# Optimization experiments

Hardware: AMD Instinct MI355X
Metric: run time of the kernel (lower is better)

The kernel has to match this reference:

```python
import jax, jax.numpy as jnp
import numpy as np

D_MODEL = 1024
NUM_HEADS = 16
HEAD_DIM = D_MODEL // NUM_HEADS
NUM_KERNELS = 21


def tisa_bias(amp, off, sharp, seq_len):
    # amp/off/sharp: (H, K). Returns (H, L, L) translation-invariant bias.
    # Evaluate on the 2L-1 distinct relative distances, then gather (Toeplitz).
    d = jnp.arange(-(seq_len - 1), seq_len, dtype=amp.dtype)  # (2L-1,)
    # (H, K, 2L-1) -> sum over kernels -> (H, 2L-1)
    scores = jnp.sum(
        amp[:, :, None]
        * jnp.exp(-jnp.abs(sharp)[:, :, None] * (d[None, None, :] - off[:, :, None]) ** 2),
        axis=1,
    )
    i = jnp.arange(seq_len)
    rel_idx = i[None, :] - i[:, None] + (seq_len - 1)  # (L, L) in [0, 2L-2]
    return scores[:, rel_idx]  # (H, L, L)


def setup_inputs() -> dict:
    key = jax.random.key(0)
    ks = jax.random.split(key, 9)
    B, L = 4, 1024
    s = 0.02
    return {
        "x_q": jax.random.normal(ks[0], (B, L, D_MODEL), dtype=jnp.float32),
        "x_kv": jax.random.normal(ks[1], (B, L, D_MODEL), dtype=jnp.float32),
        "Wq": jax.random.normal(ks[2], (D_MODEL, D_MODEL), dtype=jnp.float32) * s,
        "Wm": jax.random.normal(ks[3], (D_MODEL, 2 * D_MODEL), dtype=jnp.float32) * s,
        "Wg": jax.random.normal(ks[4], (D_MODEL, 2 * D_MODEL), dtype=jnp.float32) * s,
        "bg": jnp.zeros((2 * D_MODEL,), dtype=jnp.float32),
        "tisa_amp": jax.random.normal(ks[5], (NUM_HEADS, NUM_KERNELS), dtype=jnp.float32) * 0.1,
        "tisa_off": jax.random.uniform(ks[6], (NUM_HEADS, NUM_KERNELS), dtype=jnp.float32, minval=-512.0, maxval=512.0),
        "tisa_sharp": jax.random.uniform(ks[7], (NUM_HEADS, NUM_KERNELS), dtype=jnp.float32, minval=1e-4, maxval=0.05),
    }


def reference(x_q, x_kv, Wq, Wm, Wg, bg, tisa_amp, tisa_off, tisa_sharp):
    B, Lq, _ = x_q.shape
    Lkv = x_kv.shape[1]
    H, Dh = NUM_HEADS, HEAD_DIM

    q = (x_q @ Wq).reshape(B, Lq, H, Dh).transpose(0, 2, 1, 3)        # (B,H,Lq,Dh)
    mem = (x_kv @ Wm)                                                 # (B,Lkv,2D)
    k = mem[..., :D_MODEL].reshape(B, Lkv, H, Dh).transpose(0, 2, 1, 3)
    v = mem[..., D_MODEL:].reshape(B, Lkv, H, Dh).transpose(0, 2, 1, 3)

    scale = 1.0 / jnp.sqrt(jnp.asarray(Dh, dtype=q.dtype))
    scores = jnp.einsum("bhqd,bhkd->bhqk", q, k) * scale              # (B,H,Lq,Lkv)
    scores = scores + tisa_bias(tisa_amp, tisa_off, tisa_sharp, Lkv)[None]
    weights = jax.nn.softmax(scores, axis=-1)

    attn = jnp.einsum("bhqk,bhkd->bhqd", weights, v)                  # (B,H,Lq,Dh)
    attn = attn.transpose(0, 2, 1, 3).reshape(B, Lq, D_MODEL)

    g = attn @ Wg + bg                                                # (B,Lq,2D)
    a, b = g[..., :D_MODEL], g[..., D_MODEL:]
    return a * jax.nn.sigmoid(b)
```

## Files before the change

kernel.cpp:

```cpp
#include <hip/hip_runtime.h>
#include <cstdint>
#include <cstddef>

typedef __attribute__((ext_vector_type(8))) short bf16x8;
typedef __attribute__((ext_vector_type(4))) float f32x4;

#define LOG2E 1.44269504f

__device__ __forceinline__ unsigned short f2bf(float x) {
  unsigned int u = __float_as_uint(x);
  u += 0x7FFFu + ((u >> 16) & 1u);
  return (unsigned short)(u >> 16);
}
__device__ __forceinline__ unsigned short f2bf_trunc(float x) {
  return (unsigned short)(__float_as_uint(x) >> 16);
}

__device__ __forceinline__ void gload_lds16(const void* g, void* l) {
  __builtin_amdgcn_global_load_lds(
      (const __attribute__((address_space(1))) unsigned int*)g,
      (__attribute__((address_space(3))) unsigned int*)l, 16, 0, 0);
}


__global__ void preproc(const float* __restrict__ x_q, const float* __restrict__ x_kv,
                        const float* __restrict__ Wq, const float* __restrict__ Wm,
                        const float* __restrict__ Wg,
                        const float* __restrict__ amp, const float* __restrict__ off,
                        const float* __restrict__ sharp,
                        ushort4* __restrict__ bXq, ushort4* __restrict__ bXkv,
                        unsigned short* __restrict__ dWq, unsigned short* __restrict__ dWm,
                        unsigned short* __restrict__ dWg, float* __restrict__ tab) {
  __shared__ float tile[32][33];
  const int blk = blockIdx.x;
  if (blk < 8192) {
    int i = blk * 256 + threadIdx.x;
    float4 v;
    ushort4* d;
    if (i < (1 << 20)) { v = ((const float4*)x_q)[i]; d = bXq + i; }
    else { int j = i - (1 << 20); v = ((const float4*)x_kv)[j]; d = bXkv + j; }
    ushort4 o;
    o.x = f2bf(v.x); o.y = f2bf(v.y); o.z = f2bf(v.z); o.w = f2bf(v.w);
    *d = o;
  } else if (blk < 14336) {
    int idx = blk - 8192;
    int z = idx >> 11, rem = idx & 2047;
    int bx = rem & 63, by = rem >> 6;
    const float* src = z == 0 ? Wq : (z == 1 ? Wm : Wg);
    unsigned short* dst = z == 0 ? dWq : (z == 1 ? dWm : dWg);
    int N = z == 0 ? 1024 : 2048;
    int nb = bx * 32, kb = by * 32;
    if (nb >= N) return;
    int tx = threadIdx.x & 31, ty = threadIdx.x >> 5;
#pragma unroll
    for (int r = ty; r < 32; r += 8)
      tile[r][tx] = src[(size_t)(kb + r) * N + nb + tx];
    __syncthreads();
#pragma unroll
    for (int r = ty; r < 32; r += 8)
      dst[(size_t)(nb + r) * 1024 + kb + tx] = f2bf(tile[tx][r]);
  } else {
    int h = blk - 14336;
    for (int idx = threadIdx.x; idx < 2047; idx += 256) {
      float d = (float)(idx - 1023);
      float acc = 0.f;
#pragma unroll
      for (int k = 0; k < 21; ++k) {
        float dd = d - off[h * 21 + k];
        acc += amp[h * 21 + k] * __expf(-fabsf(sharp[h * 21 + k]) * dd * dd);
      }
      tab[h * 2047 + idx] = acc * LOG2E;
    }
  }
}


__global__ __launch_bounds__(256)
void qkv_gemm(const unsigned short* __restrict__ Xq,
              const unsigned short* __restrict__ Xkv,
              const unsigned short* __restrict__ WqT,
              const unsigned short* __restrict__ WmT,
              unsigned short* __restrict__ qbuf,
              unsigned short* __restrict__ kbuf,
              unsigned short* __restrict__ vtbuf) {
  __shared__ unsigned short sA[2][128 * 32];
  __shared__ unsigned short sB[2][128 * 32];
  const int bx = blockIdx.y;
  const bool isQ = bx < 8;
  const int ntile = (isQ ? bx : bx - 8) << 7;
  const unsigned short* A = isQ ? Xq : Xkv;
  const unsigned short* B = (isQ ? WqT : WmT) + (size_t)ntile * 1024;
  const int t = threadIdx.x, lane = t & 63, w = t >> 6;
  const int wm = (w >> 1) << 6, wn = (w & 1) << 6;
  const int mtile = blockIdx.x << 7;
  const int c = lane & 15, g = lane >> 4;
  const int srow = t >> 2, scol = (t & 3) << 3;
  const unsigned short* aP = A + (size_t)(mtile + srow) * 1024 + scol;
  const unsigned short* bP = B + (size_t)srow * 1024 + scol;
  const int lo = srow * 32 + scol;

  gload_lds16(aP, &sA[0][lo]);
  gload_lds16(aP + 64 * 1024, &sA[0][lo + 64 * 32]);
  gload_lds16(bP, &sB[0][lo]);
  gload_lds16(bP + 64 * 1024, &sB[0][lo + 64 * 32]);
  __syncthreads();

  f32x4 acc[4][4] = {};
  for (int kt = 0; kt < 32; ++kt) {
    const int cur = kt & 1;
    if (kt + 1 < 32) {
      const int ko = (kt + 1) * 32;
      gload_lds16(aP + ko, &sA[1 - cur][lo]);
      gload_lds16(aP + 64 * 1024 + ko, &sA[1 - cur][lo + 64 * 32]);
      gload_lds16(bP + ko, &sB[1 - cur][lo]);
      gload_lds16(bP + 64 * 1024 + ko, &sB[1 - cur][lo + 64 * 32]);
    }
    bf16x8 af[4], bfr[4];
#pragma unroll
    for (int i = 0; i < 4; ++i) {
      af[i]  = *(const bf16x8*)&sA[cur][(wm + i * 16 + c) * 32 + g * 8];
      bfr[i] = *(const bf16x8*)&sB[cur][(wn + i * 16 + c) * 32 + g * 8];
    }
#pragma unroll
    for (int i = 0; i < 4; ++i)
#pragma unroll
      for (int j = 0; j < 4; ++j)
        acc[i][j] = __builtin_amdgcn_mfma_f32_16x16x32_bf16(af[i], bfr[j], acc[i][j], 0, 0, 0);
    __syncthreads();
  }

  const int row0 = mtile + wm + (g << 2);
  const int col0 = ntile + wn + c;
  if (isQ) {
#pragma unroll
    for (int i = 0; i < 4; ++i)
#pragma unroll
      for (int j = 0; j < 4; ++j) {
        int r = row0 + i * 16, cl = col0 + j * 16;
#pragma unroll
        for (int ri = 0; ri < 4; ++ri)
          qbuf[(size_t)(r + ri) * 1024 + cl] = f2bf(acc[i][j][ri] * (0.125f * LOG2E));
      }
  } else {
#pragma unroll
    for (int i = 0; i < 4; ++i)
#pragma unroll
      for (int j = 0; j < 4; ++j) {
        int r = row0 + i * 16, cl = col0 + j * 16;
        if (cl < 1024) {
#pragma unroll
          for (int ri = 0; ri < 4; ++ri)
            kbuf[(size_t)(r + ri) * 1024 + cl] = f2bf(acc[i][j][ri]);
        } else {
          int d = cl - 1024;
          int hh = d >> 6, dh = d & 63;
          int bb = r >> 10, ll = r & 1023;
          ushort4 pk;
          pk.x = f2bf(acc[i][j][0]);
          pk.y = f2bf(acc[i][j][1]);
          pk.z = f2bf(acc[i][j][2]);
          pk.w = f2bf(acc[i][j][3]);
          *(ushort4*)&vtbuf[((size_t)((bb * 16 + hh) * 64 + dh) << 10) + ll] = pk;
        }
      }
  }
}


__global__ __launch_bounds__(512)
void attn_kernel(const unsigned short* __restrict__ qbuf,
                 const unsigned short* __restrict__ kbuf,
                 const unsigned short* __restrict__ vtbuf,
                 const float* __restrict__ biasTab,
                 unsigned short* __restrict__ attnb) {
  const int h = blockIdx.x & 15, b = blockIdx.x >> 4, qt = blockIdx.y;
  __shared__ unsigned short sK[2][64 * 64];
  __shared__ unsigned short sV[3][64 * 64];
  __shared__ unsigned short sP[2][128 * 64];
  __shared__ float sLsum[2][128];
  const int t = threadIdx.x, lane = t & 63, w = t >> 6;
  const int c = lane & 15, g = lane >> 4;
  const int rg = w >> 1, cg = w & 1;

  const int r = t >> 3, ch = (t & 7) ^ (r & 7);

  const unsigned short* qsrc = qbuf + (size_t)(b * 1024 + qt * 128) * 1024 + h * 64;
  const unsigned short* ksrc = kbuf + (size_t)(b * 1024) * 1024 + h * 64;
  const unsigned short* vsrc = vtbuf + (size_t)((b * 16 + h) * 64) * 1024;

  unsigned short* sQ = &sP[0][0];
  gload_lds16(qsrc + (size_t)r * 1024 + ch * 8, &sQ[t * 8]);
  gload_lds16(qsrc + (size_t)(r + 64) * 1024 + ch * 8, &sQ[4096 + t * 8]);
  gload_lds16(ksrc + (size_t)r * 1024 + ch * 8, &sK[0][t * 8]);
  gload_lds16(vsrc + (size_t)r * 1024 + ch * 8, &sV[0][t * 8]);

  const float* bb = biasTab + h * 2047 + 1023 + cg * 32 + c - qt * 128 - rg * 32 - g * 4;

  float bc[2][2][4];
#pragma unroll
  for (int rf = 0; rf < 2; ++rf)
#pragma unroll
    for (int nf = 0; nf < 2; ++nf)
#pragma unroll
      for (int ri = 0; ri < 4; ++ri)
        bc[rf][nf][ri] = bb[(nf - rf) * 16 - ri];

  __syncthreads();

  bf16x8 aq[2][2];
#pragma unroll
  for (int rf = 0; rf < 2; ++rf) {
    int row = rg * 32 + rf * 16 + c;
#pragma unroll
    for (int ks = 0; ks < 2; ++ks)
      aq[rf][ks] = *(const bf16x8*)&sQ[row * 64 + (((ks * 4 + g) ^ (row & 7)) * 8)];
  }
  __syncthreads();

  f32x4 o[2][2] = {};
  float lsum[2][4] = {};

  int vcur = 0, vnx = 1;
  for (int kv = 0; kv < 16; ++kv) {
    const int cur = kv & 1;

    f32x4 s[2][2];
#pragma unroll
    for (int rf = 0; rf < 2; ++rf)
#pragma unroll
      for (int nf = 0; nf < 2; ++nf)
#pragma unroll
        for (int ri = 0; ri < 4; ++ri)
          s[rf][nf][ri] = bc[rf][nf][ri];

    if (kv + 1 < 16) {
      gload_lds16(ksrc + (size_t)((kv + 1) * 64 + r) * 1024 + ch * 8, &sK[1 - cur][t * 8]);
      gload_lds16(vsrc + (size_t)r * 1024 + (kv + 1) * 64 + ch * 8, &sV[vnx][t * 8]);
      const float* bk = bb + (kv + 1) * 64;
#pragma unroll
      for (int rf = 0; rf < 2; ++rf)
#pragma unroll
        for (int nf = 0; nf < 2; ++nf)
#pragma unroll
          for (int ri = 0; ri < 4; ++ri)
            bc[rf][nf][ri] = bk[(nf - rf) * 16 - ri];
    }

#pragma unroll
    for (int nf = 0; nf < 2; ++nf) {
      int krow = cg * 32 + nf * 16 + c;
      bf16x8 k0 = *(const bf16x8*)&sK[cur][krow * 64 + (((g) ^ (krow & 7)) * 8)];
      bf16x8 k1 = *(const bf16x8*)&sK[cur][krow * 64 + (((4 + g) ^ (krow & 7)) * 8)];
#pragma unroll
      for (int rf = 0; rf < 2; ++rf) {
        s[rf][nf] = __builtin_amdgcn_mfma_f32_16x16x32_bf16(aq[rf][0], k0, s[rf][nf], 0, 0, 0);
        s[rf][nf] = __builtin_amdgcn_mfma_f32_16x16x32_bf16(aq[rf][1], k1, s[rf][nf], 0, 0, 0);
      }
    }

#pragma unroll
    for (int rf = 0; rf < 2; ++rf)
#pragma unroll
      for (int nf = 0; nf < 2; ++nf)
#pragma unroll
        for (int ri = 0; ri < 4; ++ri) {
          float e = exp2f(s[rf][nf][ri]);
          lsum[rf][ri] += e;
          int prow = rg * 32 + rf * 16 + g * 4 + ri;
          int chunk = cg * 4 + nf * 2 + (c >> 3);
          sP[cur][prow * 64 + ((chunk ^ (prow & 7)) * 8) + (c & 7)] = f2bf_trunc(e);
        }
    __syncthreads();

    bf16x8 ap[2][2];
#pragma unroll
    for (int rf = 0; rf < 2; ++rf) {
      int row = rg * 32 + rf * 16 + c;
#pragma unroll
      for (int ks = 0; ks < 2; ++ks)
        ap[rf][ks] = *(const bf16x8*)&sP[cur][row * 64 + (((ks * 4 + g) ^ (row & 7)) * 8)];
    }
#pragma unroll
    for (int df = 0; df < 2; ++df) {
      int vrow = cg * 32 + df * 16 + c;
      bf16x8 v0 = *(const bf16x8*)&sV[vcur][vrow * 64 + (((g) ^ (vrow & 7)) * 8)];
      bf16x8 v1 = *(const bf16x8*)&sV[vcur][vrow * 64 + (((4 + g) ^ (vrow & 7)) * 8)];
#pragma unroll
      for (int rf = 0; rf < 2; ++rf) {
        o[rf][df] = __builtin_amdgcn_mfma_f32_16x16x32_bf16(ap[rf][0], v0, o[rf][df], 0, 0, 0);
        o[rf][df] = __builtin_amdgcn_mfma_f32_16x16x32_bf16(ap[rf][1], v1, o[rf][df], 0, 0, 0);
      }
    }
    vcur = vnx;
    vnx = (vnx == 2) ? 0 : vnx + 1;
  }

#pragma unroll
  for (int off = 1; off < 16; off <<= 1)
#pragma unroll
    for (int rf = 0; rf < 2; ++rf)
#pragma unroll
      for (int ri = 0; ri < 4; ++ri)
        lsum[rf][ri] += __shfl_xor(lsum[rf][ri], off, 64);
  if (c == 0) {
#pragma unroll
    for (int rf = 0; rf < 2; ++rf)
#pragma unroll
      for (int ri = 0; ri < 4; ++ri)
        sLsum[cg][rg * 32 + rf * 16 + g * 4 + ri] = lsum[rf][ri];
  }
  __syncthreads();

  unsigned short* obase = attnb +
      (size_t)(b * 1024 + qt * 128 + rg * 32 + g * 4) * 1024 + h * 64 + cg * 32 + c;
#pragma unroll
  for (int rf = 0; rf < 2; ++rf)
#pragma unroll
    for (int ri = 0; ri < 4; ++ri) {
      int row = rg * 32 + rf * 16 + g * 4 + ri;
      float rinv = 1.0f / (sLsum[0][row] + sLsum[1][row]);
#pragma unroll
      for (int df = 0; df < 2; ++df)
        obase[(size_t)(rf * 16 + ri) * 1024 + df * 16] = f2bf(o[rf][df][ri] * rinv);
    }
}


__global__ __launch_bounds__(256, 4)
void out_gemm(const unsigned short* __restrict__ A,
              const unsigned short* __restrict__ WgT,
              const float* __restrict__ bg,
              float* __restrict__ out) {
  __shared__ unsigned short sA[2][64 * 32];
  __shared__ unsigned short sB[2][128 * 32];
  const int nb = blockIdx.y;
  const int mtile = blockIdx.x << 6;
  const int t = threadIdx.x, lane = t & 63, w = t >> 6;
  const int c = lane & 15, g = lane >> 4;
  const int rm = w >> 1, cn = w & 1;
  const int srow = t >> 2, scol = (t & 3) << 3;
  const unsigned short* aP = A + (size_t)(mtile + srow) * 1024 + scol;
  const unsigned short* bP0 = WgT + (size_t)(nb * 64 + srow) * 1024 + scol;
  const unsigned short* bP1 = WgT + (size_t)(1024 + nb * 64 + srow) * 1024 + scol;
  const int lo = srow * 32 + scol;

  gload_lds16(aP, &sA[0][lo]);
  gload_lds16(bP0, &sB[0][lo]);
  gload_lds16(bP1, &sB[0][lo + 64 * 32]);
  __syncthreads();

  f32x4 acc[2][4] = {};
  for (int kt = 0; kt < 32; ++kt) {
    const int cur = kt & 1;
    if (kt + 1 < 32) {
      const int ko = (kt + 1) * 32;
      gload_lds16(aP + ko, &sA[1 - cur][lo]);
      gload_lds16(bP0 + ko, &sB[1 - cur][lo]);
      gload_lds16(bP1 + ko, &sB[1 - cur][lo + 64 * 32]);
    }
    bf16x8 af[2], bfr[4];
#pragma unroll
    for (int i = 0; i < 2; ++i)
      af[i] = *(const bf16x8*)&sA[cur][(rm * 32 + i * 16 + c) * 32 + g * 8];
#pragma unroll
    for (int jj = 0; jj < 2; ++jj) {
      bfr[jj]     = *(const bf16x8*)&sB[cur][(cn * 32 + jj * 16 + c) * 32 + g * 8];
      bfr[jj + 2] = *(const bf16x8*)&sB[cur][(64 + cn * 32 + jj * 16 + c) * 32 + g * 8];
    }
#pragma unroll
    for (int i = 0; i < 2; ++i)
#pragma unroll
      for (int j = 0; j < 4; ++j)
        acc[i][j] = __builtin_amdgcn_mfma_f32_16x16x32_bf16(af[i], bfr[j], acc[i][j], 0, 0, 0);
    __syncthreads();
  }

#pragma unroll
  for (int i = 0; i < 2; ++i) {
    int row0 = mtile + rm * 32 + i * 16 + (g << 2);
#pragma unroll
    for (int jj = 0; jj < 2; ++jj) {
      int col = nb * 64 + cn * 32 + jj * 16 + c;
      float ba = bg[col];
      float bbv = bg[1024 + col];
#pragma unroll
      for (int ri = 0; ri < 4; ++ri) {
        float av = acc[i][jj][ri] + ba;
        float bv = acc[i][jj + 2][ri] + bbv;
        out[(size_t)(row0 + ri) * 1024 + col] = av / (1.f + exp2f(-LOG2E * bv));
      }
    }
  }
}


extern "C" void kernel_launch(void* const* d_in, const int* in_sizes, int n_in,
                              void* d_out, int out_size, void* d_ws, size_t ws_size,
                              hipStream_t stream) {
  const float* x_q   = (const float*)d_in[0];
  const float* x_kv  = (const float*)d_in[1];
  const float* Wq    = (const float*)d_in[2];
  const float* Wm    = (const float*)d_in[3];
  const float* Wg    = (const float*)d_in[4];
  const float* bg    = (const float*)d_in[5];
  const float* amp   = (const float*)d_in[6];
  const float* off   = (const float*)d_in[7];
  const float* sharp = (const float*)d_in[8];
  float* out = (float*)d_out;

  char* ws = (char*)d_ws;
  size_t o = 0;
  auto alloc = [&](size_t bytes) {
    char* p = ws + o;
    o += (bytes + 255) & ~(size_t)255;
    return p;
  };
  unsigned short* bXq   = (unsigned short*)alloc(4096ull * 1024 * 2);
  unsigned short* bXkv  = (unsigned short*)alloc(4096ull * 1024 * 2);
  unsigned short* bWqT  = (unsigned short*)alloc(1024ull * 1024 * 2);
  unsigned short* bWmT  = (unsigned short*)alloc(2048ull * 1024 * 2);
  unsigned short* bWgT  = (unsigned short*)alloc(2048ull * 1024 * 2);
  float*          biasT = (float*)alloc(16ull * 2047 * 4);
  unsigned short* qbuf  = (unsigned short*)alloc(4096ull * 1024 * 2);
  unsigned short* kbuf  = (unsigned short*)alloc(4096ull * 1024 * 2);
  unsigned short* vtbuf = (unsigned short*)alloc(4096ull * 1024 * 2);
  unsigned short* attnb = (unsigned short*)alloc(4096ull * 1024 * 2);
  if (ws_size < o) return;

  preproc<<<14352, 256, 0, stream>>>(x_q, x_kv, Wq, Wm, Wg, amp, off, sharp,
                                     (ushort4*)bXq, (ushort4*)bXkv,
                                     bWqT, bWmT, bWgT, biasT);
  qkv_gemm<<<dim3(32, 24), 256, 0, stream>>>(bXq, bXkv, bWqT, bWmT, qbuf, kbuf, vtbuf);
  attn_kernel<<<dim3(64, 8), 512, 0, stream>>>(qbuf, kbuf, vtbuf, biasT, attnb);
  out_gemm<<<dim3(64, 16), 256, 0, stream>>>(attnb, bWgT, bg, out);
}
```

Measured before the change: 210.1 us.

## Enlarge QKV GEMM tiles to 256x256x64 with swizzled LDS and split-phase pipelining

The QKV projection GEMM moves from 128x128 tiles with K-step 32 and 256 threads to 256x256 tiles with K-step 64 and 512 threads. LDS writes use an XOR swizzle to avoid bank conflicts. Each K-step is split into two MFMA phases, and the next tile's global-to-LDS loads are issued between them under explicit waitcnt, barriers and setprio. The aim is more data reuse per block and better overlap of loads with MFMA work. The cost is only 192 blocks, which may underfill the GPU's CUs, plus more LDS (128KB) and register pressure.

```diff
diff --git a/kernel.cpp b/kernel.cpp
--- a/kernel.cpp
+++ b/kernel.cpp
@@ -75,7 +75,7 @@
 }
 
 
-__global__ __launch_bounds__(256)
+__global__ __launch_bounds__(512, 2)
 void qkv_gemm(const unsigned short* __restrict__ Xq,
               const unsigned short* __restrict__ Xkv,
               const unsigned short* __restrict__ WqT,
@@ -83,57 +83,101 @@
               unsigned short* __restrict__ qbuf,
               unsigned short* __restrict__ kbuf,
               unsigned short* __restrict__ vtbuf) {
-  __shared__ unsigned short sA[2][128 * 32];
-  __shared__ unsigned short sB[2][128 * 32];
-  const int bx = blockIdx.y;
-  const bool isQ = bx < 8;
-  const int ntile = (isQ ? bx : bx - 8) << 7;
+  __shared__ unsigned short sA[2][256 * 64];
+  __shared__ unsigned short sB[2][256 * 64];
+  const int y = blockIdx.y;
+  const bool isQ = y < 4;
+  const int ntile = (isQ ? y : y - 4) << 8;
   const unsigned short* A = isQ ? Xq : Xkv;
-  const unsigned short* B = (isQ ? WqT : WmT) + (size_t)ntile * 1024;
+  const unsigned short* Bp = (isQ ? WqT : WmT) + (size_t)ntile * 1024;
+  const int mtile = blockIdx.x << 8;
   const int t = threadIdx.x, lane = t & 63, w = t >> 6;
-  const int wm = (w >> 1) << 6, wn = (w & 1) << 6;
-  const int mtile = blockIdx.x << 7;
+  const int wm = w >> 2, wn = w & 3;
   const int c = lane & 15, g = lane >> 4;
-  const int srow = t >> 2, scol = (t & 3) << 3;
-  const unsigned short* aP = A + (size_t)(mtile + srow) * 1024 + scol;
-  const unsigned short* bP = B + (size_t)srow * 1024 + scol;
-  const int lo = srow * 32 + scol;
-
-  gload_lds16(aP, &sA[0][lo]);
-  gload_lds16(aP + 64 * 1024, &sA[0][lo + 64 * 32]);
-  gload_lds16(bP, &sB[0][lo]);
-  gload_lds16(bP + 64 * 1024, &sB[0][lo + 64 * 32]);
-  __syncthreads();
-
-  f32x4 acc[4][4] = {};
-  for (int kt = 0; kt < 32; ++kt) {
-    const int cur = kt & 1;
-    if (kt + 1 < 32) {
-      const int ko = (kt + 1) * 32;
-      gload_lds16(aP + ko, &sA[1 - cur][lo]);
-      gload_lds16(aP + 64 * 1024 + ko, &sA[1 - cur][lo + 64 * 32]);
-      gload_lds16(bP + ko, &sB[1 - cur][lo]);
-      gload_lds16(bP + 64 * 1024 + ko, &sB[1 - cur][lo + 64 * 32]);
-    }
-    bf16x8 af[4], bfr[4];
-#pragma unroll
-    for (int i = 0; i < 4; ++i) {
-      af[i]  = *(const bf16x8*)&sA[cur][(wm + i * 16 + c) * 32 + g * 8];
-      bfr[i] = *(const bf16x8*)&sB[cur][(wn + i * 16 + c) * 32 + g * 8];
-    }
-#pragma unroll
-    for (int i = 0; i < 4; ++i)
+
+  const int tr = t >> 3;
+  const int tc = (t & 7) ^ (tr & 7);
+  const unsigned short* aP = A + (size_t)(mtile + tr) * 1024 + tc * 8;
+  const unsigned short* bP = Bp + (size_t)tr * 1024 + tc * 8;
+  const int lo = tr * 64 + (t & 7) * 8;
+
+#pragma unroll
+  for (int i = 0; i < 4; ++i) {
+    gload_lds16(aP + (size_t)(i * 64) * 1024, &sA[0][lo + i * 4096]);
+    gload_lds16(bP + (size_t)(i * 64) * 1024, &sB[0][lo + i * 4096]);
+  }
+#pragma unroll
+  for (int i = 0; i < 4; ++i) {
+    gload_lds16(aP + (size_t)(i * 64) * 1024 + 64, &sA[1][lo + i * 4096]);
+    gload_lds16(bP + (size_t)(i * 64) * 1024 + 64, &sB[1][lo + i * 4096]);
+  }
+  asm volatile("s_waitcnt vmcnt(8)" ::: "memory");
+  asm volatile("s_barrier" ::: "memory");
+
+  const int sw0 = (g ^ (c & 7)) * 8;
+  const int sw1 = ((4 + g) ^ (c & 7)) * 8;
+  const int arow = (wm * 128 + c) * 64;
+  const int brow = (wn * 64 + c) * 64;
+
+  f32x4 acc[8][4] = {};
+
+  for (int kt = 0; kt < 16; ++kt) {
+    const unsigned short* sAp = sA[kt & 1];
+    const unsigned short* sBc = sB[kt & 1];
+
+    bf16x8 a0[8], b0[4];
+#pragma unroll
+    for (int i = 0; i < 8; ++i) a0[i] = *(const bf16x8*)&sAp[arow + i * 1024 + sw0];
+#pragma unroll
+    for (int j = 0; j < 4; ++j) b0[j] = *(const bf16x8*)&sBc[brow + j * 1024 + sw0];
+    __builtin_amdgcn_s_setprio(1);
+#pragma unroll
+    for (int i = 0; i < 8; ++i)
 #pragma unroll
       for (int j = 0; j < 4; ++j)
-        acc[i][j] = __builtin_amdgcn_mfma_f32_16x16x32_bf16(af[i], bfr[j], acc[i][j], 0, 0, 0);
-    __syncthreads();
-  }
-
-  const int row0 = mtile + wm + (g << 2);
-  const int col0 = ntile + wn + c;
+        acc[i][j] = __builtin_amdgcn_mfma_f32_16x16x32_bf16(a0[i], b0[j], acc[i][j], 0, 0, 0);
+    __builtin_amdgcn_s_setprio(0);
+
+    bf16x8 a1[8], b1[4];
+#pragma unroll
+    for (int i = 0; i < 8; ++i) a1[i] = *(const bf16x8*)&sAp[arow + i * 1024 + sw1];
+#pragma unroll
+    for (int j = 0; j < 4; ++j) b1[j] = *(const bf16x8*)&sBc[brow + j * 1024 + sw1];
+    asm volatile("s_waitcnt lgkmcnt(0)" ::: "memory");
+    asm volatile("s_barrier" ::: "memory");
+
+    if (kt < 14) {
+      const unsigned short* aPk = aP + (kt + 2) * 64;
+      const unsigned short* bPk = bP + (kt + 2) * 64;
+#pragma unroll
+      for (int i = 0; i < 4; ++i) {
+        gload_lds16(aPk + (size_t)(i * 64) * 1024, &sA[kt & 1][lo + i * 4096]);
+        gload_lds16(bPk + (size_t)(i * 64) * 1024, &sB[kt & 1][lo + i * 4096]);
+      }
+    }
+    __builtin_amdgcn_sched_barrier(0);
+
+    __builtin_amdgcn_s_setprio(1);
+#pragma unroll
+    for (int i = 0; i < 8; ++i)
+#pragma unroll
+      for (int j = 0; j < 4; ++j)
+        acc[i][j] = __builtin_amdgcn_mfma_f32_16x16x32_bf16(a1[i], b1[j], acc[i][j], 0, 0, 0);
+    __builtin_amdgcn_s_setprio(0);
+    __builtin_amdgcn_sched_barrier(0);
+
+    if (kt < 14)
+      asm volatile("s_waitcnt vmcnt(8)" ::: "memory");
+    else
+      asm volatile("s_waitcnt vmcnt(0)" ::: "memory");
+    asm volatile("s_barrier" ::: "memory");
+  }
+
+  const int row0 = mtile + wm * 128 + (g << 2);
+  const int col0 = ntile + wn * 64 + c;
   if (isQ) {
 #pragma unroll
-    for (int i = 0; i < 4; ++i)
+    for (int i = 0; i < 8; ++i)
 #pragma unroll
       for (int j = 0; j < 4; ++j) {
         int r = row0 + i * 16, cl = col0 + j * 16;
@@ -141,27 +185,31 @@
         for (int ri = 0; ri < 4; ++ri)
           qbuf[(size_t)(r + ri) * 1024 + cl] = f2bf(acc[i][j][ri] * (0.125f * LOG2E));
       }
-  } else {
-#pragma unroll
-    for (int i = 0; i < 4; ++i)
+  } else if (ntile < 1024) {
+#pragma unroll
+    for (int i = 0; i < 8; ++i)
 #pragma unroll
       for (int j = 0; j < 4; ++j) {
         int r = row0 + i * 16, cl = col0 + j * 16;
-        if (cl < 1024) {
-#pragma unroll
-          for (int ri = 0; ri < 4; ++ri)
-            kbuf[(size_t)(r + ri) * 1024 + cl] = f2bf(acc[i][j][ri]);
-        } else {
-          int d = cl - 1024;
-          int hh = d >> 6, dh = d & 63;
-          int bb = r >> 10, ll = r & 1023;
-          ushort4 pk;
-          pk.x = f2bf(acc[i][j][0]);
-          pk.y = f2bf(acc[i][j][1]);
-          pk.z = f2bf(acc[i][j][2]);
-          pk.w = f2bf(acc[i][j][3]);
-          *(ushort4*)&vtbuf[((size_t)((bb * 16 + hh) * 64 + dh) << 10) + ll] = pk;
-        }
+#pragma unroll
+        for (int ri = 0; ri < 4; ++ri)
+          kbuf[(size_t)(r + ri) * 1024 + cl] = f2bf(acc[i][j][ri]);
+      }
+  } else {
+#pragma unroll
+    for (int i = 0; i < 8; ++i)
+#pragma unroll
+      for (int j = 0; j < 4; ++j) {
+        int r = row0 + i * 16, cl = col0 + j * 16;
+        int d = cl - 1024;
+        int hh = d >> 6, dh = d & 63;
+        int bb2 = r >> 10, ll = r & 1023;
+        ushort4 pk;
+        pk.x = f2bf(acc[i][j][0]);
+        pk.y = f2bf(acc[i][j][1]);
+        pk.z = f2bf(acc[i][j][2]);
+        pk.w = f2bf(acc[i][j][3]);
+        *(ushort4*)&vtbuf[((size_t)((bb2 * 16 + hh) * 64 + dh) << 10) + ll] = pk;
       }
   }
 }
@@ -430,7 +478,7 @@
   preproc<<<14352, 256, 0, stream>>>(x_q, x_kv, Wq, Wm, Wg, amp, off, sharp,
                                      (ushort4*)bXq, (ushort4*)bXkv,
                                      bWqT, bWmT, bWgT, biasT);
-  qkv_gemm<<<dim3(32, 24), 256, 0, stream>>>(bXq, bXkv, bWqT, bWmT, qbuf, kbuf, vtbuf);
+  qkv_gemm<<<dim3(16, 12), 512, 0, stream>>>(bXq, bXkv, bWqT, bWmT, qbuf, kbuf, vtbuf);
   attn_kernel<<<dim3(64, 8), 512, 0, stream>>>(qbuf, kbuf, vtbuf, biasT, attnb);
   out_gemm<<<dim3(64, 16), 256, 0, stream>>>(attnb, bWgT, bg, out);
 }
```

Result: no change. 209.3 us (-0.4%).
